# Kernel optimization log

Hardware: AMD Instinct MI355X
Metric: run time of the kernel (lower is better)

## Reference

```python
import jax, jax.numpy as jnp
import numpy as np

STRIDE = 16
SCALES = (0.5, 1.0, 2.0)
RATIOS = (0.5, 1.0, 2.0)
IOU_THR = 0.7
CONF_THR = 0.5
KEEP_PRE = 6000
KEEP_POST = 300


def _default_boxes(fh, fw):
    # anchors centered at origin: size = stride*scale, w/h set by aspect ratio
    s = STRIDE * jnp.asarray(SCALES, jnp.float32)                    # [S]
    r = jnp.asarray(RATIOS, jnp.float32)                             # [R]
    w = (s[None, :] * jnp.sqrt(1.0 / r)[:, None]).reshape(-1)        # [A]
    h = (s[None, :] * jnp.sqrt(r)[:, None]).reshape(-1)              # [A]
    anchors = jnp.stack([-w / 2, -h / 2, w / 2, h / 2], axis=-1)     # [A,4]
    sx = jnp.arange(fw, dtype=jnp.float32) * STRIDE
    sy = jnp.arange(fh, dtype=jnp.float32) * STRIDE
    gx, gy = jnp.meshgrid(sx, sy)                                    # [fh,fw]
    shifts = jnp.stack([gx, gy, gx, gy], axis=-1)                    # [fh,fw,4]
    return (shifts[:, :, None, :] + anchors[None, None, :, :]).reshape(-1, 4)


def _apply_regs(deltas, boxes):
    # deltas: [bs,N,4] (dx,dy,dw,dh); boxes: [N,4] xyxy default boxes
    w = boxes[:, 2] - boxes[:, 0]
    h = boxes[:, 3] - boxes[:, 1]
    cx = boxes[:, 0] + 0.5 * w
    cy = boxes[:, 1] + 0.5 * h
    pcx = deltas[..., 0] * w + cx
    pcy = deltas[..., 1] * h + cy
    pw = jnp.exp(deltas[..., 2]) * w
    ph = jnp.exp(deltas[..., 3]) * h
    return jnp.stack([pcx - 0.5 * pw, pcy - 0.5 * ph,
                      pcx + 0.5 * pw, pcy + 0.5 * ph], axis=-1)


def _clip(boxes, img_h, img_w):
    lim = jnp.asarray([img_w, img_h, img_w, img_h], jnp.float32)
    return jnp.clip(boxes, 0.0, lim)


def _pairwise_iou(b):
    area = jnp.maximum(b[:, 2] - b[:, 0], 0.0) * jnp.maximum(b[:, 3] - b[:, 1], 0.0)
    lt = jnp.maximum(b[:, None, :2], b[None, :, :2])
    rb = jnp.minimum(b[:, None, 2:], b[None, :, 2:])
    wh = jnp.maximum(rb - lt, 0.0)
    inter = wh[..., 0] * wh[..., 1]
    union = area[:, None] + area[None, :] - inter
    return inter / jnp.maximum(union, 1e-9)


def _nms_keep(boxes, thr):
    # boxes are pre-sorted by descending score -> greedy NMS == row sweep
    n = boxes.shape[0]
    iou = _pairwise_iou(jax.lax.stop_gradient(boxes))  # [n,n]
    idx = jnp.arange(n)
    def body(i, keep):
        sup = (iou[i] > thr) & (idx > i)
        return keep & jnp.where(keep[i], ~sup, True)
    return jax.lax.fori_loop(0, n, body, jnp.ones(n, dtype=bool))


def _detect_one(boxes, scores):
    order = jnp.argsort(-scores)
    props = boxes[order][:KEEP_PRE]          # [P,4]
    sc = scores[order][:KEEP_PRE]            # [P]
    keep = _nms_keep(props, IOU_THR)
    pos = jnp.cumsum(keep) - 1               # compacted position of kept boxes
    valid = keep & (pos < KEEP_POST)
    dst = jnp.where(valid, pos, KEEP_POST)   # out-of-range -> dropped by scatter
    out_b = jnp.zeros((KEEP_POST, 4), props.dtype).at[dst].set(props, mode='drop')
    out_s = jnp.zeros((KEEP_POST,), sc.dtype).at[dst].set(sc, mode='drop')
    # confidence filter: zero out rows below threshold (fixed-shape analog of list)
    return out_b * (out_s > CONF_THR).astype(props.dtype)[:, None]


def reference(preds, regs, img_h, img_w):
    bs, fh, fw, na = preds.shape
    db = _default_boxes(fh, fw)                          # [fh*fw*A, 4]
    scores = jax.nn.sigmoid(preds).reshape(bs, -1)       # [bs, N]
    boxes = _apply_regs(regs.reshape(bs, -1, 4), db)     # [bs, N, 4]
    boxes = _clip(boxes, img_h, img_w)
    outs = [_detect_one(boxes[i], scores[i]) for i in range(bs)]
    return jnp.stack(outs)                               # [bs, KEEP_POST, 4]


def setup_inputs() -> dict:
    key = jax.random.key(0)
    k1, k2 = jax.random.split(key)
    preds = jax.random.normal(k1, (4, 37, 62, 9), jnp.float32)
    regs = jax.random.normal(k2, (4, 37, 62, 9, 4), jnp.float32)
    return {"preds": preds, "regs": regs, "img_h": 600, "img_w": 1000}
```

## Files before the change

kernel.cpp:

```cpp
#include <hip/hip_runtime.h>
#include <stdint.h>

typedef unsigned long long u64;
typedef unsigned int u32;

#define FH 37
#define FW 62
#define NA 9
#define NPRED 20646
#define BS 4
#define KEEP_PRE 6000
#define KEEP_POST 300
#define NBINS 4096
#define SELCAP 3072
#define SLOTN 6144
#define FB_BASE 4608
#define NFB 640
#define NCHUNK 21
#define FSLOTS 32
#define FSUB 128

#define L_HIST   0u
#define L_SUF    16384u
#define L_FINEH  32768u
#define L_FINES  49152u
#define L_FINEC  65536u
#define L_FBCUR  81920u
#define L_SLOTS  84480u
#define L_PERM   133632u
#define L_KBOX   145920u
#define L_KAREA  150720u
#define L_WSUM   151920u
#define L_WPOS   151984u
#define L_SCAL   152048u
#define LDS_TOTAL 152064u
#define L_CBOX   32768u

__device__ __forceinline__ u32 mapbits(float p) {
  u32 u = __float_as_uint(p);
  return (u & 0x80000000u) ? ~u : (u | 0x80000000u);
}
__device__ __forceinline__ float bcast(float v, int srcLane) {
  return __int_as_float(__builtin_amdgcn_readlane(__float_as_int(v), srcLane));
}
__device__ __forceinline__ bool iou_sup(float kx1, float ky1, float kx2, float ky2,
                                        float ka, float cx1, float cy1,
                                        float cx2, float cy2, float ca) {
  float wx = fmaxf(fminf(kx2, cx2) - fmaxf(kx1, cx1), 0.f);
  float wy = fmaxf(fminf(ky2, cy2) - fmaxf(ky1, cy1), 0.f);
  float inter = wx * wy;
  float un = ka + ca - inter;
  return inter > 0.7f * fmaxf(un, 1e-9f);
}
__device__ __forceinline__ float4 decode_box(u32 n, float4 d, float W, float H) {
  int a = (int)(n % NA);
  int cell = (int)(n / NA);
  int x = cell % FW;
  int y = cell / FW;
  int si = a % 3, ri = a / 3;
  float s = (si==0) ? 8.f : ((si==1) ? 16.f : 32.f);
  float r = (ri==0) ? 0.5f : ((ri==1) ? 1.0f : 2.0f);
  float aw = s * sqrtf(1.0f / r);
  float ah = s * sqrtf(r);
  float gx = (float)x * 16.f, gy = (float)y * 16.f;
  float x1d = gx - 0.5f*aw, x2d = gx + 0.5f*aw;
  float y1d = gy - 0.5f*ah, y2d = gy + 0.5f*ah;
  float w = x2d - x1d, h = y2d - y1d;
  float cx = x1d + 0.5f*w, cy = y1d + 0.5f*h;
  float pcx = d.x*w + cx, pcy = d.y*h + cy;
  float pw = expf(d.z)*w, ph = expf(d.w)*h;
  float bx1 = fminf(fmaxf(pcx - 0.5f*pw, 0.f), W);
  float by1 = fminf(fmaxf(pcy - 0.5f*ph, 0.f), H);
  float bx2 = fminf(fmaxf(pcx + 0.5f*pw, 0.f), W);
  float by2 = fminf(fmaxf(pcy + 0.5f*ph, 0.f), H);
  return make_float4(bx1, by1, bx2, by2);
}

__device__ __forceinline__ void suffix_scan4096(const u32* h, u32* suf, u32* cur,
                                                u32* wsum, int t, int lane, int wv) {
  u32 h0 = h[4*t], h1 = h[4*t+1], h2 = h[4*t+2], h3 = h[4*t+3];
  u32 s = h0 + h1 + h2 + h3;
  u32 sf = s;
  #pragma unroll
  for (int off = 1; off < 64; off <<= 1) {
    u32 o = __shfl_down(sf, off, 64);
    if (lane + off < 64) sf += o;
  }
  if (lane == 0) wsum[wv] = sf;
  __syncthreads();
  u32 hi = 0;
  for (int w2 = wv + 1; w2 < 16; ++w2) hi += wsum[w2];
  u32 St = hi + (sf - s);
  u32 s3 = St, s2 = s3 + h3, s1 = s2 + h2, s0 = s1 + h1;
  suf[4*t] = s0; suf[4*t+1] = s1; suf[4*t+2] = s2; suf[4*t+3] = s3;
  if (cur) { cur[4*t] = s0; cur[4*t+1] = s1; cur[4*t+2] = s2; cur[4*t+3] = s3; }
}

__global__ void __launch_bounds__(1024, 4) detect_kernel(
    const float* __restrict__ preds, const float4* __restrict__ regs4,
    const int* __restrict__ ih, const int* __restrict__ iw,
    float4* __restrict__ out)
{
  __shared__ __align__(16) char smem[LDS_TOTAL];
  u32*    histL   = (u32*)(smem + L_HIST);
  u32*    sufL    = (u32*)(smem + L_SUF);
  u32*    fineH   = (u32*)(smem + L_FINEH);
  u32*    fineSuf = (u32*)(smem + L_FINES);
  u32*    fineCur = (u32*)(smem + L_FINEC);
  u32*    fbCur   = (u32*)(smem + L_FBCUR);
  u64*    slots   = (u64*)(smem + L_SLOTS);
  u32*    perm    = (u32*)(smem + L_PERM);
  float4* kbox    = (float4*)(smem + L_KBOX);
  float*  karea   = (float*)(smem + L_KAREA);
  u32*    wsum    = (u32*)(smem + L_WSUM);
  u32*    wpos    = (u32*)(smem + L_WPOS);
  u32*    scal    = (u32*)(smem + L_SCAL);
  float4* cbox    = (float4*)(smem + L_CBOX);

  const int b = blockIdx.x;
  const int t = threadIdx.x;
  const int lane = t & 63;
  const int wv = t >> 6;
  const float* pb = preds + b*NPRED;
  const float4* rb = regs4 + b*NPRED;
  const float W = (float)(*iw), H = (float)(*ih);

  #pragma unroll
  for (int q = 0; q < 4; ++q) histL[q*1024 + t] = 0;
  if (t == 0) scal[2] = 0;
  __syncthreads();

  float pv[NCHUNK];
  #pragma unroll
  for (int c = 0; c < NCHUNK; ++c) {
    int n = c*1024 + t;
    pv[c] = (n < NPRED) ? pb[n] : -__builtin_inff();
  }
  {
    u32 mypos = 0;
    #pragma unroll
    for (int c = 0; c < NCHUNK; ++c) {
      int n = c*1024 + t;
      bool valid = (n < NPRED);
      u64 bm = __ballot(valid && (pv[c] > 0.0f));
      mypos += (u32)__popcll(bm);
      u32 m = mapbits(pv[c]);
      if (valid) atomicAdd(&histL[m >> 20], 1u);
    }
    if (lane == 0) wpos[wv] = mypos;
  }
  __syncthreads();

  suffix_scan4096(histL, sufL, nullptr, wsum, t, lane, wv);
  if (t == 0) {
    u32 np = 0;
    #pragma unroll
    for (int w2 = 0; w2 < 16; ++w2) np += wpos[w2];
    scal[3] = np;
  }
  __syncthreads();

  #pragma unroll 1
  for (int tr = 0; tr < 2; ++tr) {
    const u32 winStart = (u32)tr * SELCAP;
    const u32 winEnd = winStart + SELCAP;
    const int rowLimit = (KEEP_PRE - (int)winStart < (int)SELCAP)
                           ? (KEEP_PRE - (int)winStart) : (int)SELCAP;

    if (t == 0) { scal[0] = 0xFFFFFFFFu; scal[1] = 0u; }
    __syncthreads();
    #pragma unroll
    for (int q = 0; q < 4; ++q) {
      int v = 4*t + q;
      u32 hv = histL[v], sv = sufL[v];
      if (hv && sv < winEnd && sv + hv > winStart) {
        atomicMin(&scal[0], (u32)v);
        atomicMax(&scal[1], (u32)v);
      }
    }
    __syncthreads();
    const u32 binLo = scal[0], binHi = scal[1];
    u32 cBase = binLo;
    if (binHi - binLo >= FSLOTS) cBase = binHi - (FSLOTS - 1);
    const u32 S_top = sufL[binHi];
    const u32 S_cb = (cBase > 0) ? sufL[cBase-1] : 0;
    const u32 rebWinEnd = winEnd - S_top;

    #pragma unroll
    for (int q = 0; q < 4; ++q) fineH[q*1024 + t] = 0;
    #pragma unroll
    for (int q = 0; q < 6; ++q) slots[q*1024 + t] = 0ull;
    if (t < NFB) {
      u32 v = binLo + (u32)t;
      fbCur[t] = (v < cBase) ? (FB_BASE + (sufL[v] - S_cb)) : (u32)SLOTN;
    }
    __syncthreads();

    #pragma unroll
    for (int c = 0; c < NCHUNK; ++c) {
      int n = c*1024 + t;
      if (n < NPRED) {
        u32 m = mapbits(pv[c]);
        u32 cb = m >> 20;
        if (cb >= cBase && cb <= binHi)
          atomicAdd(&fineH[((cb - cBase) << 7) | ((m >> 13) & 0x7F)], 1u);
      }
    }
    __syncthreads();
    suffix_scan4096(fineH, fineSuf, fineCur, wsum, t, lane, wv);
    __syncthreads();

    #pragma unroll
    for (int c = 0; c < NCHUNK; ++c) {
      int n = c*1024 + t;
      if (n < NPRED) {
        u32 m = mapbits(pv[c]);
        u32 cb = m >> 20;
        u64 key = ((u64)m << 32) | (u32)(~(u32)n);
        if (cb >= cBase && cb <= binHi) {
          u32 F = ((cb - cBase) << 7) | ((m >> 13) & 0x7F);
          if (fineSuf[F] < rebWinEnd) {
            u32 pos = atomicAdd(&fineCur[F], 1u);
            if (pos < FB_BASE) slots[pos] = key;
          }
        } else if (cb >= binLo && cb < cBase) {
          u32 fo = cb - binLo;
          if (fo < NFB) {
            u32 pos = atomicAdd(&fbCur[fo], 1u);
            if (pos < SLOTN) slots[pos] = key;
          }
        }
      }
    }
    __syncthreads();

    #pragma unroll
    for (int q = 0; q < 6; ++q) {
      int i = q*1024 + t;
      u64 k = slots[i];
      if (k != 0) {
        u32 m = (u32)(k >> 32);
        u32 cb = m >> 20;
        u32 rank;
        if (cb >= cBase) {
          u32 F = ((cb - cBase) << 7) | ((m >> 13) & 0x7F);
          u32 base = fineSuf[F];
          u32 end = base + fineH[F]; if (end > FB_BASE) end = FB_BASE;
          u32 c2 = 0;
          for (u32 j = base; j < end; ++j) c2 += (slots[j] > k) ? 1u : 0u;
          rank = S_top + fineSuf[F] + c2;
        } else {
          u32 base = FB_BASE + (sufL[cb] - S_cb);
          u32 end = base + histL[cb]; if (end > SLOTN) end = SLOTN;
          u32 c2 = 0;
          for (u32 j = base; j < end; ++j) c2 += (slots[j] > k) ? 1u : 0u;
          rank = sufL[cb] + c2;
        }
        int local = (int)rank - (int)winStart;
        if (local >= 0 && local < rowLimit) perm[local] = ~(u32)k;
      }
    }
    __syncthreads();

    for (int r = t; r < rowLimit; r += 1024) {
      u32 idx = perm[r];
      float4 d = rb[idx];
      cbox[r] = decode_box(idx, d, W, H);
    }
    __syncthreads();

    if (wv == 0) {
      int cnt = (int)scal[2];
      const int npos = (int)scal[3];
      float4* ob = out + b*KEEP_POST;
      const float4 zero = make_float4(0.f, 0.f, 0.f, 0.f);
      const int nblk = (rowLimit + 63) >> 6;

      for (int blk = 0; blk < nblk && cnt < KEEP_POST; ++blk) {
        const int base = blk * 64;
        const int ci = base + lane;
        float4 cur = cbox[(ci < rowLimit) ? ci : 0];
        float carea = (cur.z - cur.x) * (cur.w - cur.y);

        asm volatile("s_waitcnt lgkmcnt(0)" ::: "memory");

        int dead = 0;
        {
          int k = 0;
          for (; k + 8 <= cnt; k += 8) {
            float4 b0 = kbox[k+0], b1 = kbox[k+1], b2 = kbox[k+2], b3 = kbox[k+3];
            float4 b4 = kbox[k+4], b5 = kbox[k+5], b6 = kbox[k+6], b7 = kbox[k+7];
            float a0 = karea[k+0], a1 = karea[k+1], a2 = karea[k+2], a3 = karea[k+3];
            float a4 = karea[k+4], a5 = karea[k+5], a6 = karea[k+6], a7 = karea[k+7];
            dead |= (int)iou_sup(b0.x,b0.y,b0.z,b0.w,a0, cur.x,cur.y,cur.z,cur.w,carea);
            dead |= (int)iou_sup(b1.x,b1.y,b1.z,b1.w,a1, cur.x,cur.y,cur.z,cur.w,carea);
            dead |= (int)iou_sup(b2.x,b2.y,b2.z,b2.w,a2, cur.x,cur.y,cur.z,cur.w,carea);
            dead |= (int)iou_sup(b3.x,b3.y,b3.z,b3.w,a3, cur.x,cur.y,cur.z,cur.w,carea);
            dead |= (int)iou_sup(b4.x,b4.y,b4.z,b4.w,a4, cur.x,cur.y,cur.z,cur.w,carea);
            dead |= (int)iou_sup(b5.x,b5.y,b5.z,b5.w,a5, cur.x,cur.y,cur.z,cur.w,carea);
            dead |= (int)iou_sup(b6.x,b6.y,b6.z,b6.w,a6, cur.x,cur.y,cur.z,cur.w,carea);
            dead |= (int)iou_sup(b7.x,b7.y,b7.z,b7.w,a7, cur.x,cur.y,cur.z,cur.w,carea);
          }
          for (; k < cnt; ++k) {
            float4 kb = kbox[k];
            dead |= (int)iou_sup(kb.x,kb.y,kb.z,kb.w,karea[k],
                                 cur.x,cur.y,cur.z,cur.w,carea);
          }
        }
        bool alive = (ci < rowLimit) && !dead;
        u64 A = __ballot((int)alive);

        while (A && cnt < KEEP_POST) {
          int j = (int)__builtin_ctzll(A);
          A &= A - 1;
          float jx1 = bcast(cur.x, j), jy1 = bcast(cur.y, j);
          float jx2 = bcast(cur.z, j), jy2 = bcast(cur.w, j);
          float ja  = bcast(carea, j);
          bool sup = iou_sup(jx1, jy1, jx2, jy2, ja,
                             cur.x, cur.y, cur.z, cur.w, carea);
          u64 S = __ballot((int)sup);
          A &= ~S;
          if (lane == 0) {
            float4 bj = make_float4(jx1, jy1, jx2, jy2);
            kbox[cnt] = bj;
            karea[cnt] = ja;
            ob[cnt] = ((int)(winStart + (u32)(base + j)) < npos) ? bj : zero;
          }
          ++cnt;
        }
      }
      if (lane == 0) scal[2] = (u32)cnt;
    }
    __syncthreads();
    if ((int)scal[2] >= KEEP_POST) break;
  }

  if (wv == 0) {
    float4* ob = out + b*KEEP_POST;
    const float4 zero = make_float4(0.f, 0.f, 0.f, 0.f);
    for (int k2 = (int)scal[2] + lane; k2 < KEEP_POST; k2 += 64) ob[k2] = zero;
  }
}

extern "C" void kernel_launch(void* const* d_in, const int* in_sizes, int n_in,
                              void* d_out, int out_size, void* d_ws, size_t ws_size,
                              hipStream_t stream) {
  const float* preds  = (const float*)d_in[0];
  const float4* regs4 = (const float4*)d_in[1];
  const int* ih       = (const int*)d_in[2];
  const int* iw       = (const int*)d_in[3];
  (void)d_ws; (void)ws_size; (void)in_sizes; (void)n_in; (void)out_size;

  detect_kernel<<<dim3(BS), 1024, 0, stream>>>(
      preds, regs4, ih, iw, (float4*)d_out);
}
```

Baseline: 200.6 us.

## Parallelize NMS across all waves and replicate histograms to cut contention

The NMS phase now spreads the check of each 64-candidate block against already-kept boxes across all 16 waves, and precomputes the intra-block suppression masks in parallel, leaving only a short bitmask sweep to wave 0. The coarse histogram is split into four replicas to reduce LDS atomic contention, and the fine histogram is halved to 2048 bins. Scores are re-read from global memory on each pass instead of being held in 21 registers, and the occupancy hint is dropped. In exchange there are two block-wide barriers per 64-row block and some repeated global loads.

```diff
diff --git a/kernel.cpp b/kernel.cpp
--- a/kernel.cpp
+++ b/kernel.cpp
@@ -18,30 +18,27 @@
 #define NFB 640
 #define NCHUNK 21
 #define FSLOTS 32
-#define FSUB 128
+#define FSUB 64
+#define NFINE 2048
 
 #define L_HIST   0u
 #define L_SUF    16384u
-#define L_FINEH  32768u
-#define L_FINES  49152u
-#define L_FINEC  65536u
-#define L_FBCUR  81920u
-#define L_SLOTS  84480u
-#define L_PERM   133632u
-#define L_KBOX   145920u
-#define L_KAREA  150720u
-#define L_WSUM   151920u
-#define L_WPOS   151984u
-#define L_SCAL   152048u
-#define LDS_TOTAL 152064u
-#define L_CBOX   32768u
+#define L_RG1    32768u
+#define L_RG2    81920u
+#define L_FBCUR  106496u
+#define L_PERM   109056u
+#define L_KBOX   121344u
+#define L_KAREA  126208u
+#define L_WSUM   127424u
+#define L_WPOS   127488u
+#define L_SCAL   127552u
+#define L_AW     127616u
+#define L_MROW   127744u
+#define LDS_TOTAL 128256u
 
 __device__ __forceinline__ u32 mapbits(float p) {
   u32 u = __float_as_uint(p);
   return (u & 0x80000000u) ? ~u : (u | 0x80000000u);
-}
-__device__ __forceinline__ float bcast(float v, int srcLane) {
-  return __int_as_float(__builtin_amdgcn_readlane(__float_as_int(v), srcLane));
 }
 __device__ __forceinline__ bool iou_sup(float kx1, float ky1, float kx2, float ky2,
                                         float ka, float cx1, float cy1,
@@ -76,46 +73,30 @@
   return make_float4(bx1, by1, bx2, by2);
 }
 
-__device__ __forceinline__ void suffix_scan4096(const u32* h, u32* suf, u32* cur,
-                                                u32* wsum, int t, int lane, int wv) {
-  u32 h0 = h[4*t], h1 = h[4*t+1], h2 = h[4*t+2], h3 = h[4*t+3];
-  u32 s = h0 + h1 + h2 + h3;
-  u32 sf = s;
-  #pragma unroll
-  for (int off = 1; off < 64; off <<= 1) {
-    u32 o = __shfl_down(sf, off, 64);
-    if (lane + off < 64) sf += o;
-  }
-  if (lane == 0) wsum[wv] = sf;
-  __syncthreads();
-  u32 hi = 0;
-  for (int w2 = wv + 1; w2 < 16; ++w2) hi += wsum[w2];
-  u32 St = hi + (sf - s);
-  u32 s3 = St, s2 = s3 + h3, s1 = s2 + h2, s0 = s1 + h1;
-  suf[4*t] = s0; suf[4*t+1] = s1; suf[4*t+2] = s2; suf[4*t+3] = s3;
-  if (cur) { cur[4*t] = s0; cur[4*t+1] = s1; cur[4*t+2] = s2; cur[4*t+3] = s3; }
-}
-
-__global__ void __launch_bounds__(1024, 4) detect_kernel(
+__global__ void __launch_bounds__(1024) detect_kernel(
     const float* __restrict__ preds, const float4* __restrict__ regs4,
     const int* __restrict__ ih, const int* __restrict__ iw,
     float4* __restrict__ out)
 {
   __shared__ __align__(16) char smem[LDS_TOTAL];
-  u32*    histL   = (u32*)(smem + L_HIST);
-  u32*    sufL    = (u32*)(smem + L_SUF);
-  u32*    fineH   = (u32*)(smem + L_FINEH);
-  u32*    fineSuf = (u32*)(smem + L_FINES);
-  u32*    fineCur = (u32*)(smem + L_FINEC);
-  u32*    fbCur   = (u32*)(smem + L_FBCUR);
-  u64*    slots   = (u64*)(smem + L_SLOTS);
-  u32*    perm    = (u32*)(smem + L_PERM);
-  float4* kbox    = (float4*)(smem + L_KBOX);
-  float*  karea   = (float*)(smem + L_KAREA);
-  u32*    wsum    = (u32*)(smem + L_WSUM);
-  u32*    wpos    = (u32*)(smem + L_WPOS);
-  u32*    scal    = (u32*)(smem + L_SCAL);
-  float4* cbox    = (float4*)(smem + L_CBOX);
+  u32*    histL  = (u32*)(smem + L_HIST);
+  u32*    sufL   = (u32*)(smem + L_SUF);
+  u32*    repl   = (u32*)(smem + L_RG1);
+  u64*    slots  = (u64*)(smem + L_RG1);
+  float4* cboxL  = (float4*)(smem + L_RG1);
+  u32*    fineH  = (u32*)(smem + L_RG2);
+  u32*    fineS  = (u32*)(smem + L_RG2 + 8192);
+  u32*    fineC  = (u32*)(smem + L_RG2 + 16384);
+  float*  careaL = (float*)(smem + L_RG2);
+  u32*    fbCur  = (u32*)(smem + L_FBCUR);
+  u32*    perm   = (u32*)(smem + L_PERM);
+  float4* kbox   = (float4*)(smem + L_KBOX);
+  float*  karea  = (float*)(smem + L_KAREA);
+  u32*    wsum   = (u32*)(smem + L_WSUM);
+  u32*    wpos   = (u32*)(smem + L_WPOS);
+  u32*    scal   = (u32*)(smem + L_SCAL);
+  u64*    aw     = (u64*)(smem + L_AW);
+  u64*    mrow   = (u64*)(smem + L_MROW);
 
   const int b = blockIdx.x;
   const int t = threadIdx.x;
@@ -124,39 +105,59 @@
   const float* pb = preds + b*NPRED;
   const float4* rb = regs4 + b*NPRED;
   const float W = (float)(*iw), H = (float)(*ih);
+  float4* ob = out + b*KEEP_POST;
+  const float4 zero = make_float4(0.f, 0.f, 0.f, 0.f);
 
   #pragma unroll
   for (int q = 0; q < 4; ++q) histL[q*1024 + t] = 0;
+  #pragma unroll
+  for (int q = 0; q < 12; ++q) repl[q*1024 + t] = 0;
   if (t == 0) scal[2] = 0;
   __syncthreads();
 
-  float pv[NCHUNK];
-  #pragma unroll
-  for (int c = 0; c < NCHUNK; ++c) {
-    int n = c*1024 + t;
-    pv[c] = (n < NPRED) ? pb[n] : -__builtin_inff();
-  }
   {
+    u32* repA = ((wv & 3) == 0) ? histL : (repl + ((wv & 3) - 1) * 4096);
     u32 mypos = 0;
-    #pragma unroll
+    #pragma unroll 4
     for (int c = 0; c < NCHUNK; ++c) {
       int n = c*1024 + t;
       bool valid = (n < NPRED);
-      u64 bm = __ballot(valid && (pv[c] > 0.0f));
+      float p = valid ? pb[n] : -1.0f;
+      u64 bm = __ballot(valid && (p > 0.0f));
       mypos += (u32)__popcll(bm);
-      u32 m = mapbits(pv[c]);
-      if (valid) atomicAdd(&histL[m >> 20], 1u);
+      if (valid) atomicAdd(&repA[mapbits(p) >> 20], 1u);
     }
     if (lane == 0) wpos[wv] = mypos;
   }
   __syncthreads();
 
-  suffix_scan4096(histL, sufL, nullptr, wsum, t, lane, wv);
-  if (t == 0) {
-    u32 np = 0;
-    #pragma unroll
-    for (int w2 = 0; w2 < 16; ++w2) np += wpos[w2];
-    scal[3] = np;
+  {
+    u32* r2 = repl + 4096; u32* r3 = repl + 8192;
+    u32 h0 = histL[4*t+0] + repl[4*t+0] + r2[4*t+0] + r3[4*t+0];
+    u32 h1 = histL[4*t+1] + repl[4*t+1] + r2[4*t+1] + r3[4*t+1];
+    u32 h2 = histL[4*t+2] + repl[4*t+2] + r2[4*t+2] + r3[4*t+2];
+    u32 h3 = histL[4*t+3] + repl[4*t+3] + r2[4*t+3] + r3[4*t+3];
+    histL[4*t+0]=h0; histL[4*t+1]=h1; histL[4*t+2]=h2; histL[4*t+3]=h3;
+    u32 s = h0 + h1 + h2 + h3;
+    u32 sf = s;
+    #pragma unroll
+    for (int off = 1; off < 64; off <<= 1) {
+      u32 o = __shfl_down(sf, off, 64);
+      if (lane + off < 64) sf += o;
+    }
+    if (lane == 0) wsum[wv] = sf;
+    __syncthreads();
+    u32 hi = 0;
+    for (int w2 = wv + 1; w2 < 16; ++w2) hi += wsum[w2];
+    u32 St = hi + (sf - s);
+    u32 s3 = St, s2 = s3 + h3, s1 = s2 + h2, s0 = s1 + h1;
+    sufL[4*t+0]=s0; sufL[4*t+1]=s1; sufL[4*t+2]=s2; sufL[4*t+3]=s3;
+    if (t == 0) {
+      u32 np = 0;
+      #pragma unroll
+      for (int w2 = 0; w2 < 16; ++w2) np += wpos[w2];
+      scal[3] = np;
+    }
   }
   __syncthreads();
 
@@ -187,7 +188,7 @@
     const u32 rebWinEnd = winEnd - S_top;
 
     #pragma unroll
-    for (int q = 0; q < 4; ++q) fineH[q*1024 + t] = 0;
+    for (int q = 0; q < 2; ++q) fineH[q*1024 + t] = 0;
     #pragma unroll
     for (int q = 0; q < 6; ++q) slots[q*1024 + t] = 0ull;
     if (t < NFB) {
@@ -196,31 +197,49 @@
     }
     __syncthreads();
 
-    #pragma unroll
+    #pragma unroll 4
     for (int c = 0; c < NCHUNK; ++c) {
       int n = c*1024 + t;
       if (n < NPRED) {
-        u32 m = mapbits(pv[c]);
+        u32 m = mapbits(pb[n]);
         u32 cb = m >> 20;
         if (cb >= cBase && cb <= binHi)
-          atomicAdd(&fineH[((cb - cBase) << 7) | ((m >> 13) & 0x7F)], 1u);
-      }
-    }
-    __syncthreads();
-    suffix_scan4096(fineH, fineSuf, fineCur, wsum, t, lane, wv);
-    __syncthreads();
-
-    #pragma unroll
+          atomicAdd(&fineH[((cb - cBase) << 6) | ((m >> 14) & 0x3F)], 1u);
+      }
+    }
+    __syncthreads();
+
+    {
+      u32 f0 = fineH[2*t], f1 = fineH[2*t+1];
+      u32 s = f0 + f1;
+      u32 sf = s;
+      #pragma unroll
+      for (int off = 1; off < 64; off <<= 1) {
+        u32 o = __shfl_down(sf, off, 64);
+        if (lane + off < 64) sf += o;
+      }
+      if (lane == 0) wsum[wv] = sf;
+      __syncthreads();
+      u32 hi = 0;
+      for (int w2 = wv + 1; w2 < 16; ++w2) hi += wsum[w2];
+      u32 St = hi + (sf - s);
+      u32 sA = St + f1, sB = St;
+      fineS[2*t] = sA; fineS[2*t+1] = sB;
+      fineC[2*t] = sA; fineC[2*t+1] = sB;
+    }
+    __syncthreads();
+
+    #pragma unroll 4
     for (int c = 0; c < NCHUNK; ++c) {
       int n = c*1024 + t;
       if (n < NPRED) {
-        u32 m = mapbits(pv[c]);
+        u32 m = mapbits(pb[n]);
         u32 cb = m >> 20;
         u64 key = ((u64)m << 32) | (u32)(~(u32)n);
         if (cb >= cBase && cb <= binHi) {
-          u32 F = ((cb - cBase) << 7) | ((m >> 13) & 0x7F);
-          if (fineSuf[F] < rebWinEnd) {
-            u32 pos = atomicAdd(&fineCur[F], 1u);
+          u32 F = ((cb - cBase) << 6) | ((m >> 14) & 0x3F);
+          if (fineS[F] < rebWinEnd) {
+            u32 pos = atomicAdd(&fineC[F], 1u);
             if (pos < FB_BASE) slots[pos] = key;
           }
         } else if (cb >= binLo && cb < cBase) {
@@ -243,12 +262,12 @@
         u32 cb = m >> 20;
         u32 rank;
         if (cb >= cBase) {
-          u32 F = ((cb - cBase) << 7) | ((m >> 13) & 0x7F);
-          u32 base = fineSuf[F];
+          u32 F = ((cb - cBase) << 6) | ((m >> 14) & 0x3F);
+          u32 base = fineS[F];
           u32 end = base + fineH[F]; if (end > FB_BASE) end = FB_BASE;
           u32 c2 = 0;
           for (u32 j = base; j < end; ++j) c2 += (slots[j] > k) ? 1u : 0u;
-          rank = S_top + fineSuf[F] + c2;
+          rank = S_top + fineS[F] + c2;
         } else {
           u32 base = FB_BASE + (sufL[cb] - S_cb);
           u32 end = base + histL[cb]; if (end > SLOTN) end = SLOTN;
@@ -264,82 +283,74 @@
 
     for (int r = t; r < rowLimit; r += 1024) {
       u32 idx = perm[r];
-      float4 d = rb[idx];
-      cbox[r] = decode_box(idx, d, W, H);
-    }
-    __syncthreads();
-
-    if (wv == 0) {
-      int cnt = (int)scal[2];
+      float4 bx = decode_box(idx, rb[idx], W, H);
+      cboxL[r] = bx;
+      careaL[r] = (bx.z - bx.x) * (bx.w - bx.y);
+    }
+    __syncthreads();
+
+    {
       const int npos = (int)scal[3];
-      float4* ob = out + b*KEEP_POST;
-      const float4 zero = make_float4(0.f, 0.f, 0.f, 0.f);
       const int nblk = (rowLimit + 63) >> 6;
-
-      for (int blk = 0; blk < nblk && cnt < KEEP_POST; ++blk) {
+      for (int blk = 0; blk < nblk; ++blk) {
+        int cnt = (int)scal[2];
+        if (cnt >= KEEP_POST) break;
         const int base = blk * 64;
         const int ci = base + lane;
-        float4 cur = cbox[(ci < rowLimit) ? ci : 0];
-        float carea = (cur.z - cur.x) * (cur.w - cur.y);
-
-        asm volatile("s_waitcnt lgkmcnt(0)" ::: "memory");
+        const bool valid = (ci < rowLimit);
+        float4 cur = cboxL[valid ? ci : 0];
+        float carea = careaL[valid ? ci : 0];
 
         int dead = 0;
-        {
-          int k = 0;
-          for (; k + 8 <= cnt; k += 8) {
-            float4 b0 = kbox[k+0], b1 = kbox[k+1], b2 = kbox[k+2], b3 = kbox[k+3];
-            float4 b4 = kbox[k+4], b5 = kbox[k+5], b6 = kbox[k+6], b7 = kbox[k+7];
-            float a0 = karea[k+0], a1 = karea[k+1], a2 = karea[k+2], a3 = karea[k+3];
-            float a4 = karea[k+4], a5 = karea[k+5], a6 = karea[k+6], a7 = karea[k+7];
-            dead |= (int)iou_sup(b0.x,b0.y,b0.z,b0.w,a0, cur.x,cur.y,cur.z,cur.w,carea);
-            dead |= (int)iou_sup(b1.x,b1.y,b1.z,b1.w,a1, cur.x,cur.y,cur.z,cur.w,carea);
-            dead |= (int)iou_sup(b2.x,b2.y,b2.z,b2.w,a2, cur.x,cur.y,cur.z,cur.w,carea);
-            dead |= (int)iou_sup(b3.x,b3.y,b3.z,b3.w,a3, cur.x,cur.y,cur.z,cur.w,carea);
-            dead |= (int)iou_sup(b4.x,b4.y,b4.z,b4.w,a4, cur.x,cur.y,cur.z,cur.w,carea);
-            dead |= (int)iou_sup(b5.x,b5.y,b5.z,b5.w,a5, cur.x,cur.y,cur.z,cur.w,carea);
-            dead |= (int)iou_sup(b6.x,b6.y,b6.z,b6.w,a6, cur.x,cur.y,cur.z,cur.w,carea);
-            dead |= (int)iou_sup(b7.x,b7.y,b7.z,b7.w,a7, cur.x,cur.y,cur.z,cur.w,carea);
+        for (int k = wv; k < cnt; k += 16) {
+          float4 kb = kbox[k];
+          dead |= (int)iou_sup(kb.x, kb.y, kb.z, kb.w, karea[k],
+                               cur.x, cur.y, cur.z, cur.w, carea);
+        }
+        aw[wv] = __ballot(dead);
+
+        #pragma unroll
+        for (int q = 0; q < 4; ++q) {
+          int j = wv*4 + q;
+          int jr = base + j; if (jr >= rowLimit) jr = 0;
+          float4 bj = cboxL[jr];
+          float ja = careaL[jr];
+          bool s = iou_sup(bj.x, bj.y, bj.z, bj.w, ja,
+                           cur.x, cur.y, cur.z, cur.w, carea);
+          u64 bm = __ballot(s);
+          if (lane == 0) mrow[j] = bm;
+        }
+        __syncthreads();
+
+        if (wv == 0) {
+          u64 deadAll = 0;
+          #pragma unroll
+          for (int k = 0; k < 16; ++k) deadAll |= aw[k];
+          int rem = rowLimit - base;
+          u64 vm = (rem >= 64) ? ~0ull : ((1ull << rem) - 1ull);
+          u64 A = vm & ~deadAll;
+          int c2 = cnt;
+          while (A && c2 < KEEP_POST) {
+            int j = (int)__builtin_ctzll(A);
+            A &= A - 1;
+            A &= ~mrow[j];
+            if (lane == 0) {
+              float4 bj = cboxL[base + j];
+              kbox[c2] = bj;
+              karea[c2] = careaL[base + j];
+              ob[c2] = ((int)(winStart + (u32)(base + j)) < npos) ? bj : zero;
+            }
+            ++c2;
           }
-          for (; k < cnt; ++k) {
-            float4 kb = kbox[k];
-            dead |= (int)iou_sup(kb.x,kb.y,kb.z,kb.w,karea[k],
-                                 cur.x,cur.y,cur.z,cur.w,carea);
-          }
-        }
-        bool alive = (ci < rowLimit) && !dead;
-        u64 A = __ballot((int)alive);
-
-        while (A && cnt < KEEP_POST) {
-          int j = (int)__builtin_ctzll(A);
-          A &= A - 1;
-          float jx1 = bcast(cur.x, j), jy1 = bcast(cur.y, j);
-          float jx2 = bcast(cur.z, j), jy2 = bcast(cur.w, j);
-          float ja  = bcast(carea, j);
-          bool sup = iou_sup(jx1, jy1, jx2, jy2, ja,
-                             cur.x, cur.y, cur.z, cur.w, carea);
-          u64 S = __ballot((int)sup);
-          A &= ~S;
-          if (lane == 0) {
-            float4 bj = make_float4(jx1, jy1, jx2, jy2);
-            kbox[cnt] = bj;
-            karea[cnt] = ja;
-            ob[cnt] = ((int)(winStart + (u32)(base + j)) < npos) ? bj : zero;
-          }
-          ++cnt;
-        }
-      }
-      if (lane == 0) scal[2] = (u32)cnt;
-    }
-    __syncthreads();
+          if (lane == 0) scal[2] = (u32)c2;
+        }
+        __syncthreads();
+      }
+    }
     if ((int)scal[2] >= KEEP_POST) break;
   }
 
-  if (wv == 0) {
-    float4* ob = out + b*KEEP_POST;
-    const float4 zero = make_float4(0.f, 0.f, 0.f, 0.f);
-    for (int k2 = (int)scal[2] + lane; k2 < KEEP_POST; k2 += 64) ob[k2] = zero;
-  }
+  for (int k2 = (int)scal[2] + t; k2 < KEEP_POST; k2 += 1024) ob[k2] = zero;
 }
 
 extern "C" void kernel_launch(void* const* d_in, const int* in_sizes, int n_in,
```

After: 172.0 us. 14.2% less time.
